# Kernel optimization log

Hardware: AMD Instinct MI355X
Metric: run time of the kernel (lower is better)

## Reference

```python
import jax, jax.numpy as jnp
import numpy as np

N_HEADS = 16
ROPE_BASE = 10000.0
EPS = float(np.finfo(np.float32).eps)  # F.rms_norm default eps for fp32


def _rms_norm(x):
    # RMSNorm over last dim, no learned scale (modded-nanogpt `norm`)
    return x * jax.lax.rsqrt(jnp.mean(jnp.square(x), axis=-1, keepdims=True) + EPS)


def _rotary(x):
    # x: [B, T, H, D]; non-interleaved half-rotation as in the Rotary module
    B, T, H, D = x.shape
    inv_freq = (1.0 / ROPE_BASE) ** (jnp.arange(0, D, 2, dtype=jnp.float32) / D)  # [D/2]
    t = jnp.arange(T, dtype=jnp.float32)
    freqs = jnp.outer(t, inv_freq)  # [T, D/2]
    cos = jnp.cos(freqs)[None, :, None, :]
    sin = jnp.sin(freqs)[None, :, None, :]
    x1, x2 = jnp.split(x, 2, axis=3)
    y1 = x1 * cos + x2 * sin
    y2 = -x1 * sin + x2 * cos
    return jnp.concatenate((y1, y2), axis=3).astype(x.dtype)


def setup_inputs() -> dict:
    key = jax.random.key(0)
    k1, k2, k3, k4 = jax.random.split(key, 4)
    B, T, Hs = 1, 2048, 2048
    d_head = Hs // N_HEADS
    std = 0.5 * d_head ** (-0.5)
    bound = 3 ** 0.5 * std
    x = jax.random.normal(k1, (B, T, Hs), dtype=jnp.float32)
    Wqkv = jax.random.uniform(k2, (3, Hs, Hs), dtype=jnp.float32, minval=-bound, maxval=bound)
    Wo_w = jax.random.normal(k3, (Hs, Hs), dtype=jnp.float32) * (Hs ** -0.5)
    Wo_b = jax.random.normal(k4, (Hs,), dtype=jnp.float32) * 0.01
    return {"x": x, "Wqkv": Wqkv, "Wo_w": Wo_w, "Wo_b": Wo_b}


def reference(x, Wqkv, Wo_w, Wo_b):
    B, T, Hs = x.shape
    d_head = Hs // N_HEADS
    # fused QKV projection: F.linear(x, Wqkv.flatten(end_dim=1)) -> x @ W^T
    W = Wqkv.reshape(3 * Hs, Hs)
    qkv = jnp.einsum('bth,oh->bto', x, W).reshape(B, T, 3 * N_HEADS, d_head)
    q, k, v = jnp.split(qkv, 3, axis=-2)  # each [B, T, H, D]
    q, k = _rms_norm(q), _rms_norm(k)
    q, k = _rotary(q), _rotary(k)
    # causal attention (flex_attention block_mask = causal), scale = 1/sqrt(d)
    scale = 1.0 / jnp.sqrt(jnp.float32(d_head))
    scores = jnp.einsum('bthd,bshd->bhts', q, k) * scale  # [B, H, T, S]
    causal = jnp.tril(jnp.ones((T, T), dtype=bool))
    scores = jnp.where(causal[None, None], scores, jnp.float32(-1e30))
    probs = jax.nn.softmax(scores, axis=-1)
    y = jnp.einsum('bhts,bshd->bthd', probs, v).reshape(B, T, Hs)
    return jnp.einsum('bth,oh->bto', y, Wo_w) + Wo_b
```

## Files before the change

kernel.cpp:

```cpp
#include <hip/hip_runtime.h>
#include <hip/hip_bf16.h>
#include <stdint.h>

#define T_SEQ 2048
#define HS    2048
#define NH    16
#define DH    128
#define QKVN  (3*HS)

typedef __attribute__((ext_vector_type(8))) short          bf16x8;
typedef __attribute__((ext_vector_type(4))) float          f32x4;
typedef __attribute__((ext_vector_type(4))) unsigned short us4;
typedef __attribute__((ext_vector_type(8))) unsigned short us8;

__device__ __forceinline__ unsigned short f2bf(float x) {
  unsigned int u = __float_as_uint(x);
  return (unsigned short)((u + 0x7fffu + ((u >> 16) & 1u)) >> 16);
}

__device__ __forceinline__ void gl_lds16(const void* g, void* l) {
  __builtin_amdgcn_global_load_lds((__attribute__((address_space(1))) void*)g,
                                   (__attribute__((address_space(3))) void*)l, 16, 0, 0);
}

__global__ __launch_bounds__(256) void cast_bf16_kernel(const float* __restrict__ in,
                                                        unsigned short* __restrict__ out, int n) {
  int i = (blockIdx.x * 256 + threadIdx.x) * 8;
  if (i >= n) return;
  f32x4 a = *(const f32x4*)(in + i);
  f32x4 b = *(const f32x4*)(in + i + 4);
  us8 r;
#pragma unroll
  for (int j = 0; j < 4; ++j) { r[j] = f2bf(a[j]); r[j + 4] = f2bf(b[j]); }
  *(us8*)(out + i) = r;
}

__global__ __launch_bounds__(256) void rope_table_kernel(float* __restrict__ cosd,
                                                         float* __restrict__ sind) {
  int i = blockIdx.x * 256 + threadIdx.x;
  if (i >= T_SEQ * 64) return;
  int t = i >> 6, f = i & 63;
  float inv = expf(-9.210340371976184f * (float)f * (1.0f / 64.0f));
  float ang = (float)t * inv;
  float s, c;
  sincosf(ang, &s, &c);
  cosd[i] = c; sind[i] = s;
}

template <int BIAS, int BN>
__global__ __launch_bounds__(256, 4)
void gemm_bt(const unsigned short* __restrict__ A, const unsigned short* __restrict__ Bt,
             float* __restrict__ C, const float* __restrict__ bias, int M, int N, int K) {
  constexpr int FN = BN / 32;
  __shared__ unsigned short As[128 * 64];
  __shared__ unsigned short Bs[BN * 64];
  const int tid  = threadIdx.x;
  const int lane = tid & 63;
  const int w    = tid >> 6;
  const int fr   = lane & 15;
  const int fq   = lane >> 4;
  const int bm   = blockIdx.y * 128;
  const int bn   = blockIdx.x * BN;
  const int wr   = (w >> 1) * 64;
  const int wc   = (w & 1) * (BN / 2);

  f32x4 acc[4][FN];
#pragma unroll
  for (int m = 0; m < 4; ++m)
#pragma unroll
    for (int n = 0; n < FN; ++n) { acc[m][n][0]=0.f; acc[m][n][1]=0.f; acc[m][n][2]=0.f; acc[m][n][3]=0.f; }

  const int srow = lane >> 3;
  const int sg   = (lane & 7) ^ srow;
  const unsigned short* Ag = A + (long)bm * K;
  const unsigned short* Bg = Bt + (long)bn * K;

  const int nk = K >> 6;
  for (int kt = 0; kt < nk; ++kt) {
    const int k0 = kt << 6;
    __syncthreads();
#pragma unroll
    for (int i = 0; i < 4; ++i) {
      int r = i * 32 + w * 8;
      gl_lds16(Ag + (long)(r + srow) * K + k0 + sg * 8, &As[r * 64]);
    }
#pragma unroll
    for (int i = 0; i < BN / 32; ++i) {
      int r = i * 32 + w * 8;
      gl_lds16(Bg + (long)(r + srow) * K + k0 + sg * 8, &Bs[r * 64]);
    }
    __syncthreads();
    __builtin_amdgcn_s_setprio(1);
#pragma unroll
    for (int ks = 0; ks < 2; ++ks) {
      bf16x8 af[4], bfr[FN];
#pragma unroll
      for (int m = 0; m < 4; ++m)
        af[m]  = *(const bf16x8*)&As[(wr + m * 16 + fr) * 64 + (((ks * 4 + fq) ^ (fr & 7)) << 3)];
#pragma unroll
      for (int n = 0; n < FN; ++n)
        bfr[n] = *(const bf16x8*)&Bs[(wc + n * 16 + fr) * 64 + (((ks * 4 + fq) ^ (fr & 7)) << 3)];
#pragma unroll
      for (int m = 0; m < 4; ++m)
#pragma unroll
        for (int n = 0; n < FN; ++n)
          acc[m][n] = __builtin_amdgcn_mfma_f32_16x16x32_bf16(af[m], bfr[n], acc[m][n], 0, 0, 0);
    }
    __builtin_amdgcn_s_setprio(0);
  }
#pragma unroll
  for (int m = 0; m < 4; ++m) {
    int row0 = bm + wr + m * 16 + fq * 4;
#pragma unroll
    for (int n = 0; n < FN; ++n) {
      int col = bn + wc + n * 16 + fr;
      float bv = BIAS ? bias[col] : 0.0f;
#pragma unroll
      for (int j = 0; j < 4; ++j)
        C[(long)(row0 + j) * N + col] = acc[m][n][j] + bv;
    }
  }
}

__global__ __launch_bounds__(256)
void normrope_qk(const float* __restrict__ qkv, const float* __restrict__ cosd,
                 const float* __restrict__ sind, unsigned short* __restrict__ qb,
                 unsigned short* __restrict__ kb) {
  const int wgl  = (blockIdx.x * 256 + threadIdx.x) >> 6;
  const int lane = threadIdx.x & 63;
  for (int rr = wgl; rr < T_SEQ * 32; rr += 4096) {
    const int t = rr >> 5;
    const int y = rr & 31;
    const float2 v = *(const float2*)(qkv + (long)t * QKVN + y * 128 + lane * 2);
    float ss = v.x * v.x + v.y * v.y;
#pragma unroll
    for (int m = 1; m < 64; m <<= 1) ss += __shfl_xor(ss, m, 64);
    const float r = rsqrtf(ss * (1.0f / 128.0f) + 1.1920928955078125e-07f);
    const float a = v.x * r, b = v.y * r;
    const float pa = __shfl_xor(a, 32, 64), pb = __shfl_xor(b, 32, 64);
    const float2 c2 = *(const float2*)(cosd + t * 64 + (lane & 31) * 2);
    const float2 s2 = *(const float2*)(sind + t * 64 + (lane & 31) * 2);
    float o0, o1;
    if (lane < 32) { o0 =  a * c2.x + pa * s2.x;  o1 =  b * c2.y + pb * s2.y; }
    else           { o0 = -pa * s2.x + a * c2.x;  o1 = -pb * s2.y + b * c2.y; }
    unsigned short* dst = (y >> 4) ? kb : qb;
    const unsigned int packed = (unsigned int)f2bf(o0) | ((unsigned int)f2bf(o1) << 16);
    *(unsigned int*)(dst + ((long)(y & 15) * T_SEQ + t) * 128 + lane * 2) = packed;
  }
}

__global__ __launch_bounds__(256)
void v_transpose(const float* __restrict__ qkv, unsigned short* __restrict__ vt) {
  const int tb = blockIdx.x;
  const int h  = blockIdx.y;
  __shared__ unsigned short vl[128][72];
  const int tid = threadIdx.x;
#pragma unroll
  for (int p = 0; p < 32; ++p) {
    int rr = p * 2 + (tid >> 7);
    int d  = tid & 127;
    float x = qkv[(long)(tb * 64 + rr) * QKVN + 2 * HS + h * 128 + d];
    vl[d][rr] = f2bf(x);
  }
  __syncthreads();
#pragma unroll
  for (int p = 0; p < 8; ++p) {
    int idx = (p * 256 + tid) * 4;
    int d = idx >> 6;
    int i = idx & 63;
    us4 val = *(const us4*)&vl[d][i];
    *(us4*)&vt[((long)h * DH + d) * T_SEQ + tb * 64 + i] = val;
  }
}

__global__ __launch_bounds__(256, 2)
void attn_kernel(const unsigned short* __restrict__ qg, const unsigned short* __restrict__ kg,
                 const unsigned short* __restrict__ vtg, float* __restrict__ accG,
                 float* __restrict__ mlG) {
  const int bi = blockIdx.x;
  const int q0 = (bi & 255) >> 4;
  const int h  = bi & 15;
  const int quarter = bi >> 8;
  const int qb = (quarter < 2) ? (31 - q0) : q0;
  const int p  = quarter & 1;
  const int slot = (qb * 16 + h) * 2 + p;

  const int kt0 = p ? ((qb >> 1) + 1) : 0;
  const int kte = p ? qb : (qb >> 1);

  const int tid = threadIdx.x, lane = tid & 63, w = tid >> 6;
  const int fr = lane & 15, fq = lane >> 4;

  float* accO = accG + (long)slot * 8192;
  float* mlO  = mlG + slot * 128;

  if (kt0 > kte) {
#pragma unroll
    for (int j3 = 0; j3 < 4; ++j3) {
      int row = w * 16 + fq * 4 + j3;
      if (fr == 0) { mlO[row] = -1e30f; mlO[64 + row] = 0.f; }
    }
    return;
  }

  __shared__ unsigned short Ks[2][64 * 128];
  __shared__ unsigned short Vts[2][128 * 64];
  __shared__ unsigned short Ps[4][16 * 72];

  const unsigned short* qh = qg  + (long)h * T_SEQ * 128;
  const unsigned short* kh = kg  + (long)h * T_SEQ * 128;
  const unsigned short* vh = vtg + (long)h * 128 * T_SEQ;

  const int krow_off = lane >> 4;
  const int vrow_off = lane >> 3;
  const int vg       = (lane & 7) ^ vrow_off;

  {
    const unsigned short* ksrc = kh + (long)kt0 * 8192;
#pragma unroll
    for (int i = 0; i < 4; ++i) {
      int c = w * 4 + i;
      int r = 4 * c + krow_off;
      int gr = (lane & 15) ^ (r & 7);
      gl_lds16(ksrc + r * 128 + gr * 8, &Ks[0][c * 512]);
    }
#pragma unroll
    for (int i = 0; i < 4; ++i) {
      int r0 = (w * 4 + i) * 8;
      gl_lds16(vh + (long)(r0 + vrow_off) * T_SEQ + kt0 * 64 + vg * 8, &Vts[0][r0 * 64]);
    }
  }

  bf16x8 aq[4];
  {
    const unsigned short* qrow = qh + (long)(qb * 64 + w * 16 + fr) * 128;
#pragma unroll
    for (int ks = 0; ks < 4; ++ks)
      aq[ks] = *(const bf16x8*)(qrow + ks * 32 + fq * 8);
  }

  bf16x8 vone;
#pragma unroll
  for (int e = 0; e < 8; ++e) vone[e] = (short)0x3F80;

  f32x4 acc[8];
#pragma unroll
  for (int n = 0; n < 8; ++n) { acc[n][0]=0.f; acc[n][1]=0.f; acc[n][2]=0.f; acc[n][3]=0.f; }
  f32x4 accS;  accS[0]=0.f; accS[1]=0.f; accS[2]=0.f; accS[3]=0.f;
  float mrow[4];
#pragma unroll
  for (int j2 = 0; j2 < 4; ++j2) mrow[j2] = -1e30f;

  const float scale2 = 0.08838834764831845f * 1.4426950408889634f;

  __syncthreads();

  for (int kt = kt0; kt <= kte; ++kt) {
    const int cur = (kt - kt0) & 1;

    if (kt < kte) {
      const int nb = cur ^ 1;
      const unsigned short* ksrc = kh + (long)(kt + 1) * 8192;
#pragma unroll
      for (int i = 0; i < 4; ++i) {
        int c = w * 4 + i;
        int r = 4 * c + krow_off;
        int gr = (lane & 15) ^ (r & 7);
        gl_lds16(ksrc + r * 128 + gr * 8, &Ks[nb][c * 512]);
      }
#pragma unroll
      for (int i = 0; i < 4; ++i) {
        int r0 = (w * 4 + i) * 8;
        gl_lds16(vh + (long)(r0 + vrow_off) * T_SEQ + (kt + 1) * 64 + vg * 8, &Vts[nb][r0 * 64]);
      }
    }

    f32x4 sv[4];
#pragma unroll
    for (int n = 0; n < 4; ++n) { sv[n][0]=0.f; sv[n][1]=0.f; sv[n][2]=0.f; sv[n][3]=0.f; }
    __builtin_amdgcn_s_setprio(1);
#pragma unroll
    for (int ks = 0; ks < 4; ++ks)
#pragma unroll
      for (int n = 0; n < 4; ++n) {
        int R = n * 16 + fr;
        bf16x8 bk = *(const bf16x8*)&Ks[cur][R * 128 + (((ks * 4 + fq) ^ (fr & 7)) << 3)];
        sv[n] = __builtin_amdgcn_mfma_f32_16x16x32_bf16(aq[ks], bk, sv[n], 0, 0, 0);
      }
    __builtin_amdgcn_s_setprio(0);

#pragma unroll
    for (int n = 0; n < 4; ++n)
#pragma unroll
      for (int j3 = 0; j3 < 4; ++j3) {
        float s = sv[n][j3] * scale2;
        if (kt == qb && (n * 16 + fr) > (w * 16 + fq * 4 + j3)) s = -1e30f;
        sv[n][j3] = s;
      }

    float pm[4];
#pragma unroll
    for (int j3 = 0; j3 < 4; ++j3)
      pm[j3] = fmaxf(fmaxf(sv[0][j3], sv[1][j3]), fmaxf(sv[2][j3], sv[3][j3]));
#pragma unroll
    for (int m = 1; m < 16; m <<= 1)
#pragma unroll
      for (int j3 = 0; j3 < 4; ++j3) pm[j3] = fmaxf(pm[j3], __shfl_xor(pm[j3], m, 64));

    bool grow = (pm[0] > mrow[0]) | (pm[1] > mrow[1]) | (pm[2] > mrow[2]) | (pm[3] > mrow[3]);
    if (__any(grow)) {
      float alpha[4];
#pragma unroll
      for (int j3 = 0; j3 < 4; ++j3) {
        float mn = fmaxf(mrow[j3], pm[j3]);
        alpha[j3] = exp2f(mrow[j3] - mn);
        mrow[j3] = mn;
      }
#pragma unroll
      for (int n = 0; n < 8; ++n)
#pragma unroll
        for (int j3 = 0; j3 < 4; ++j3) acc[n][j3] *= alpha[j3];
#pragma unroll
      for (int j3 = 0; j3 < 4; ++j3) accS[j3] *= alpha[j3];
    }

    unsigned short* pl = &Ps[w][0];
#pragma unroll
    for (int n = 0; n < 4; ++n)
#pragma unroll
      for (int j3 = 0; j3 < 4; ++j3)
        pl[(fq * 4 + j3) * 72 + n * 16 + fr] = f2bf(exp2f(sv[n][j3] - mrow[j3]));
    asm volatile("s_waitcnt lgkmcnt(0)" ::: "memory");
    __builtin_amdgcn_s_setprio(1);
#pragma unroll
    for (int ks = 0; ks < 2; ++ks) {
      bf16x8 pa = *(const bf16x8*)&pl[fr * 72 + ks * 32 + fq * 8];
      accS = __builtin_amdgcn_mfma_f32_16x16x32_bf16(pa, vone, accS, 0, 0, 0);
#pragma unroll
      for (int n = 0; n < 8; ++n) {
        int R = n * 16 + fr;
        bf16x8 bv = *(const bf16x8*)&Vts[cur][R * 64 + (((ks * 4 + fq) ^ (fr & 7)) << 3)];
        acc[n] = __builtin_amdgcn_mfma_f32_16x16x32_bf16(pa, bv, acc[n], 0, 0, 0);
      }
    }
    __builtin_amdgcn_s_setprio(0);

    __syncthreads();
  }

#pragma unroll
  for (int j3 = 0; j3 < 4; ++j3) {
    int row = w * 16 + fq * 4 + j3;
#pragma unroll
    for (int n = 0; n < 8; ++n)
      accO[row * 128 + n * 16 + fr] = acc[n][j3];
    if (fr == 0) { mlO[row] = mrow[j3]; mlO[64 + row] = accS[j3]; }
  }
}

__global__ __launch_bounds__(256)
void attn_combine(const float* __restrict__ accG, const float* __restrict__ mlG,
                  unsigned short* __restrict__ yb) {
  const int j = blockIdx.x;
  const int qb = j >> 4, h = j & 15;
  const float* a0 = accG + (long)(j * 2 + 0) * 8192;
  const float* a1 = accG + (long)(j * 2 + 1) * 8192;
  const float* ml0 = mlG + (j * 2 + 0) * 128;
  const float* ml1 = mlG + (j * 2 + 1) * 128;
  const int tid = threadIdx.x;
#pragma unroll
  for (int e = 0; e < 8; ++e) {
    int idx = e * 256 + tid;
    int row = idx >> 5;
    int c4  = (idx & 31) * 4;
    float m0 = ml0[row], l0 = ml0[64 + row];
    float m1 = ml1[row], l1 = ml1[64 + row];
    float m  = fmaxf(m0, m1);
    float w0 = exp2f(m0 - m), w1 = exp2f(m1 - m);
    float inv = 1.0f / (l0 * w0 + l1 * w1);
    f32x4 A = *(const f32x4*)(a0 + row * 128 + c4);
    f32x4 B = *(const f32x4*)(a1 + row * 128 + c4);
    us4 o;
#pragma unroll
    for (int q = 0; q < 4; ++q)
      o[q] = f2bf((A[q] * w0 + B[q] * w1) * inv);
    *(us4*)(yb + (long)(qb * 64 + row) * HS + h * 128 + c4) = o;
  }
}

extern "C" void kernel_launch(void* const* d_in, const int* in_sizes, int n_in,
                              void* d_out, int out_size, void* d_ws, size_t ws_size,
                              hipStream_t stream) {
  const float* x    = (const float*)d_in[0];
  const float* Wqkv = (const float*)d_in[1];
  const float* Wo_w = (const float*)d_in[2];
  const float* Wo_b = (const float*)d_in[3];
  float* out = (float*)d_out;
  char* ws = (char*)d_ws;

  unsigned short* xbf  = (unsigned short*)(ws + 0L);
  unsigned short* wqbf = (unsigned short*)(ws + 8388608L);
  unsigned short* wobf = (unsigned short*)(ws + 33554432L);
  float*          qkv  = (float*)         (ws + 41943040L);
  unsigned short* qb   = (unsigned short*)(ws + 92274688L);
  unsigned short* kb   = (unsigned short*)(ws + 100663296L);
  unsigned short* vt   = (unsigned short*)(ws + 109051904L);
  unsigned short* yb   = (unsigned short*)(ws + 117440512L);
  float*          cosd = (float*)         (ws + 125829120L);
  float*          sind = (float*)         (ws + 126353408L);
  float*          accG = (float*)         (ws + 0L);
  float*          mlG  = (float*)         (ws + 41943040L);

  cast_bf16_kernel<<<dim3(4194304 / 8 / 256), 256, 0, stream>>>(x, xbf, 4194304);
  cast_bf16_kernel<<<dim3(12582912 / 8 / 256), 256, 0, stream>>>(Wqkv, wqbf, 12582912);
  cast_bf16_kernel<<<dim3(4194304 / 8 / 256), 256, 0, stream>>>(Wo_w, wobf, 4194304);
  rope_table_kernel<<<dim3(512), 256, 0, stream>>>(cosd, sind);

  gemm_bt<0, 128><<<dim3(QKVN / 128, T_SEQ / 128), 256, 0, stream>>>(xbf, wqbf, qkv, nullptr,
                                                                     T_SEQ, QKVN, HS);
  normrope_qk<<<dim3(1024), 256, 0, stream>>>(qkv, cosd, sind, qb, kb);
  v_transpose<<<dim3(T_SEQ / 64, NH), 256, 0, stream>>>(qkv, vt);
  attn_kernel<<<dim3(1024), 256, 0, stream>>>(qb, kb, vt, accG, mlG);
  attn_combine<<<dim3(512), 256, 0, stream>>>(accG, mlG, yb);
  gemm_bt<1, 64><<<dim3(HS / 64, T_SEQ / 128), 256, 0, stream>>>(yb, wobf, out, Wo_b,
                                                                 T_SEQ, HS, HS);
}
```

Baseline: 296.2 us.

## Prefetch K/V tiles via registers with single LDS buffer for higher occupancy

The attention kernel drops its double-buffered LDS K/V tiles and direct global-to-LDS loads. Instead, the next tile is prefetched into registers during compute and written into a single LDS buffer after an extra barrier. Halving LDS use and raising launch bounds to 3 blocks per CU aims to increase occupancy. In exchange each iteration gets a second __syncthreads, the LDS stores now sit on the critical path, and register pressure rises, which could cause spills at the higher occupancy target.

New measurement: 295.8 us. No clear change (-0.1%).

```diff
diff --git a/kernel.cpp b/kernel.cpp
--- a/kernel.cpp
+++ b/kernel.cpp
@@ -173,7 +173,7 @@
   }
 }
 
-__global__ __launch_bounds__(256, 2)
+__global__ __launch_bounds__(256, 3)
 void attn_kernel(const unsigned short* __restrict__ qg, const unsigned short* __restrict__ kg,
                  const unsigned short* __restrict__ vtg, float* __restrict__ accG,
                  float* __restrict__ mlG) {
@@ -203,31 +203,33 @@
     return;
   }
 
-  __shared__ unsigned short Ks[2][64 * 128];
-  __shared__ unsigned short Vts[2][128 * 64];
+  __shared__ unsigned short Ks[64 * 128];
+  __shared__ unsigned short Vts[128 * 64];
   __shared__ unsigned short Ps[4][16 * 72];
 
   const unsigned short* qh = qg  + (long)h * T_SEQ * 128;
   const unsigned short* kh = kg  + (long)h * T_SEQ * 128;
   const unsigned short* vh = vtg + (long)h * 128 * T_SEQ;
 
-  const int krow_off = lane >> 4;
-  const int vrow_off = lane >> 3;
-  const int vg       = (lane & 7) ^ vrow_off;
+  us8 kreg[4], vreg[4];
 
   {
     const unsigned short* ksrc = kh + (long)kt0 * 8192;
 #pragma unroll
     for (int i = 0; i < 4; ++i) {
-      int c = w * 4 + i;
-      int r = 4 * c + krow_off;
-      int gr = (lane & 15) ^ (r & 7);
-      gl_lds16(ksrc + r * 128 + gr * 8, &Ks[0][c * 512]);
+      int gidx = tid + 256 * i;
+      int row = gidx >> 4, pos = gidx & 15;
+      kreg[i] = *(const us8*)(ksrc + row * 128 + pos * 8);
+      int d = gidx >> 3, vpos = gidx & 7;
+      vreg[i] = *(const us8*)(vh + (long)d * T_SEQ + kt0 * 64 + vpos * 8);
     }
 #pragma unroll
     for (int i = 0; i < 4; ++i) {
-      int r0 = (w * 4 + i) * 8;
-      gl_lds16(vh + (long)(r0 + vrow_off) * T_SEQ + kt0 * 64 + vg * 8, &Vts[0][r0 * 64]);
+      int gidx = tid + 256 * i;
+      int row = gidx >> 4, pos = gidx & 15;
+      *(us8*)&Ks[row * 128 + ((pos ^ (row & 7)) << 3)] = kreg[i];
+      int d = gidx >> 3, vpos = gidx & 7;
+      *(us8*)&Vts[d * 64 + ((vpos ^ (d & 7)) << 3)] = vreg[i];
     }
   }
 
@@ -256,22 +258,15 @@
   __syncthreads();
 
   for (int kt = kt0; kt <= kte; ++kt) {
-    const int cur = (kt - kt0) & 1;
-
     if (kt < kte) {
-      const int nb = cur ^ 1;
       const unsigned short* ksrc = kh + (long)(kt + 1) * 8192;
 #pragma unroll
       for (int i = 0; i < 4; ++i) {
-        int c = w * 4 + i;
-        int r = 4 * c + krow_off;
-        int gr = (lane & 15) ^ (r & 7);
-        gl_lds16(ksrc + r * 128 + gr * 8, &Ks[nb][c * 512]);
-      }
-#pragma unroll
-      for (int i = 0; i < 4; ++i) {
-        int r0 = (w * 4 + i) * 8;
-        gl_lds16(vh + (long)(r0 + vrow_off) * T_SEQ + (kt + 1) * 64 + vg * 8, &Vts[nb][r0 * 64]);
+        int gidx = tid + 256 * i;
+        int row = gidx >> 4, pos = gidx & 15;
+        kreg[i] = *(const us8*)(ksrc + row * 128 + pos * 8);
+        int d = gidx >> 3, vpos = gidx & 7;
+        vreg[i] = *(const us8*)(vh + (long)d * T_SEQ + (kt + 1) * 64 + vpos * 8);
       }
     }
 
@@ -284,7 +279,7 @@
 #pragma unroll
       for (int n = 0; n < 4; ++n) {
         int R = n * 16 + fr;
-        bf16x8 bk = *(const bf16x8*)&Ks[cur][R * 128 + (((ks * 4 + fq) ^ (fr & 7)) << 3)];
+        bf16x8 bk = *(const bf16x8*)&Ks[R * 128 + (((ks * 4 + fq) ^ (fr & 7)) << 3)];
         sv[n] = __builtin_amdgcn_mfma_f32_16x16x32_bf16(aq[ks], bk, sv[n], 0, 0, 0);
       }
     __builtin_amdgcn_s_setprio(0);
@@ -339,12 +334,23 @@
 #pragma unroll
       for (int n = 0; n < 8; ++n) {
         int R = n * 16 + fr;
-        bf16x8 bv = *(const bf16x8*)&Vts[cur][R * 64 + (((ks * 4 + fq) ^ (fr & 7)) << 3)];
+        bf16x8 bv = *(const bf16x8*)&Vts[R * 64 + (((ks * 4 + fq) ^ (fr & 7)) << 3)];
         acc[n] = __builtin_amdgcn_mfma_f32_16x16x32_bf16(pa, bv, acc[n], 0, 0, 0);
       }
     }
     __builtin_amdgcn_s_setprio(0);
 
+    __syncthreads();
+    if (kt < kte) {
+#pragma unroll
+      for (int i = 0; i < 4; ++i) {
+        int gidx = tid + 256 * i;
+        int row = gidx >> 4, pos = gidx & 15;
+        *(us8*)&Ks[row * 128 + ((pos ^ (row & 7)) << 3)] = kreg[i];
+        int d = gidx >> 3, vpos = gidx & 7;
+        *(us8*)&Vts[d * 64 + ((vpos ^ (d & 7)) << 3)] = vreg[i];
+      }
+    }
     __syncthreads();
   }
 
```
